# Performance work log

Measured on AMD Instinct MI355X. Metric: run time of the kernel, lower is better.

The kernel has to match this reference:

```python
import jax, jax.numpy as jnp
import numpy as np

BN_EPS = 1e-5
B, N, C, PART = 2, 4096, 128, 50


def _bn(h, g, b):
    # eval-mode BatchNorm1d with fresh-init running stats (mean=0, var=1)
    s = g / jnp.sqrt(1.0 + BN_EPS)
    return h * s[:, None] + b[:, None]


def _conv(w, h):
    # Conv1d kernel_size=1: [O,Cin] x [B,Cin,N] -> [B,O,N]
    return jnp.einsum('oc,bcn->bon', w, h)


def _sa(h, qk_w, v_w, v_b, t_w, t_b, g, b):
    q = _conv(qk_w, h)                       # [B,32,N]; k_conv shares q_conv weight -> k == q
    v = _conv(v_w, h) + v_b[:, None]         # [B,C,N]
    energy = jnp.einsum('bcn,bcm->bnm', q, q)  # [B,N,N]
    att = jax.nn.softmax(energy, axis=-1)
    att = att / (1e-9 + att.sum(axis=1, keepdims=True))  # L1 renorm over columns
    x_r = jnp.einsum('bcn,bnm->bcm', v, att)  # [B,C,N]
    x_r = jax.nn.relu(_bn(_conv(t_w, h - x_r) + t_b[:, None], g, b))
    return h + x_r


def setup_inputs() -> dict:
    key = jax.random.key(0)
    ks = jax.random.split(key, 16)
    d = {
        'x': jax.random.normal(ks[0], (B, N, 3), jnp.float32),
        'cls_label': jax.random.uniform(ks[1], (B, 16, 1), jnp.float32),
        'conv1_w': jax.random.normal(ks[2], (128, 3), jnp.float32) * 0.3,
        'bn1_g': jnp.ones((128,), jnp.float32), 'bn1_b': jnp.zeros((128,), jnp.float32),
        'conv2_w': jax.random.normal(ks[3], (128, 128), jnp.float32) * 0.08,
        'bn2_g': jnp.ones((128,), jnp.float32), 'bn2_b': jnp.zeros((128,), jnp.float32),
        'sa_qk_w': jax.random.normal(ks[4], (4, 32, 128), jnp.float32) * 0.08,
        'sa_v_w': jax.random.normal(ks[5], (4, 128, 128), jnp.float32) * 0.08,
        'sa_v_b': jnp.zeros((4, 128), jnp.float32),
        'sa_t_w': jax.random.normal(ks[6], (4, 128, 128), jnp.float32) * 0.08,
        'sa_t_b': jnp.zeros((4, 128), jnp.float32),
        'sa_bn_g': jnp.ones((4, 128), jnp.float32), 'sa_bn_b': jnp.zeros((4, 128), jnp.float32),
        'fuse_w': jax.random.normal(ks[7], (1024, 512), jnp.float32) * 0.04,
        'fuse_bn_g': jnp.ones((1024,), jnp.float32), 'fuse_bn_b': jnp.zeros((1024,), jnp.float32),
        'label_w': jax.random.normal(ks[8], (64, 16), jnp.float32) * 0.25,
        'label_bn_g': jnp.ones((64,), jnp.float32), 'label_bn_b': jnp.zeros((64,), jnp.float32),
        'convs1_w': jax.random.normal(ks[9], (512, 3136), jnp.float32) * 0.018,
        'convs1_b': jnp.zeros((512,), jnp.float32),
        'bns1_g': jnp.ones((512,), jnp.float32), 'bns1_b': jnp.zeros((512,), jnp.float32),
        'convs2_w': jax.random.normal(ks[10], (256, 512), jnp.float32) * 0.04,
        'convs2_b': jnp.zeros((256,), jnp.float32),
        'bns2_g': jnp.ones((256,), jnp.float32), 'bns2_b': jnp.zeros((256,), jnp.float32),
        'convs3_w': jax.random.normal(ks[11], (50, 256), jnp.float32) * 0.06,
        'convs3_b': jnp.zeros((50,), jnp.float32),
    }
    return d


def reference(x, cls_label, conv1_w, bn1_g, bn1_b, conv2_w, bn2_g, bn2_b,
              sa_qk_w, sa_v_w, sa_v_b, sa_t_w, sa_t_b, sa_bn_g, sa_bn_b,
              fuse_w, fuse_bn_g, fuse_bn_b, label_w, label_bn_g, label_bn_b,
              convs1_w, convs1_b, bns1_g, bns1_b, convs2_w, convs2_b, bns2_g, bns2_b,
              convs3_w, convs3_b):
    h = jnp.transpose(x, (0, 2, 1))                      # [B,3,N]
    h = jax.nn.relu(_bn(_conv(conv1_w, h), bn1_g, bn1_b))
    h = jax.nn.relu(_bn(_conv(conv2_w, h), bn2_g, bn2_b))
    feats = []
    for i in range(4):
        h = _sa(h, sa_qk_w[i], sa_v_w[i], sa_v_b[i], sa_t_w[i], sa_t_b[i], sa_bn_g[i], sa_bn_b[i])
        feats.append(h)
    h = jnp.concatenate(feats, axis=1)                   # [B,512,N]
    h = jax.nn.leaky_relu(_bn(_conv(fuse_w, h), fuse_bn_g, fuse_bn_b), 0.2)  # [B,1024,N]
    x_max = jnp.max(h, axis=2, keepdims=True)            # [B,1024,1]
    x_avg = jnp.mean(h, axis=2, keepdims=True)
    cls_f = jax.nn.leaky_relu(_bn(_conv(label_w, cls_label), label_bn_g, label_bn_b), 0.2)  # [B,64,1]
    n = h.shape[2]
    glob = jnp.concatenate([
        jnp.broadcast_to(x_max, (h.shape[0], 1024, n)),
        jnp.broadcast_to(x_avg, (h.shape[0], 1024, n)),
        jnp.broadcast_to(cls_f, (h.shape[0], 64, n)),
    ], axis=1)
    h = jnp.concatenate([h, glob], axis=1)               # [B,3136,N]
    h = jax.nn.relu(_bn(_conv(convs1_w, h) + convs1_b[:, None], bns1_g, bns1_b))
    # dropout is identity in eval mode
    h = jax.nn.relu(_bn(_conv(convs2_w, h) + convs2_b[:, None], bns2_g, bns2_b))
    h = _conv(convs3_w, h) + convs3_b[:, None]           # [B,50,N]
    return h
```

## Files before the change

### kernel.cpp

```cpp
#include <hip/hip_runtime.h>

#define NP 4096
#define BB 2

typedef __attribute__((ext_vector_type(8))) short short8;
typedef __attribute__((ext_vector_type(4))) float f32x4;
#define MFMA_BF16 __builtin_amdgcn_mfma_f32_16x16x32_bf16

__device__ __forceinline__ float wsum(float v){
  #pragma unroll
  for (int o = 32; o; o >>= 1) v += __shfl_down(v, o, 64);
  return v;
}
__device__ __forceinline__ unsigned short f2bf(float x){
  unsigned int u = __float_as_uint(x);
  return (unsigned short)((u + 0x7fffu + ((u >> 16) & 1u)) >> 16);
}
__device__ __forceinline__ float bfh(unsigned short h){
  return __uint_as_float((unsigned int)h << 16);
}
__device__ __forceinline__ float bf2f(unsigned short h, unsigned short l){
  return bfh(h) + bfh(l);
}
__device__ __forceinline__ short8 ld8(const unsigned short* p){
  return *(const short8*)p;
}

__global__ __launch_bounds__(256) void k_wsplit(
    const float* __restrict__ src, size_t src_ls,
    unsigned short* __restrict__ dh, unsigned short* __restrict__ dl,
    size_t dst_ls, int O, int O_span, int O_pad, int o_base, int Cin, int ldsrc)
{
  const int y = blockIdx.y;
  const int idx = blockIdx.x * 256 + threadIdx.x;
  const int chunks = (Cin >> 6) * O_span * 8;
  if (idx >= chunks) return;
  const int qs = idx & 7;
  const int ol = (idx >> 3) % O_span;
  const int cc = idx / (8 * O_span);
  const int od = o_base + ol;
  short8 vh = {0,0,0,0,0,0,0,0}, vl = {0,0,0,0,0,0,0,0};
  if (ol < O) {
    const float* sp = src + (size_t)y * src_ls + (size_t)ol * ldsrc
                    + cc * 64 + ((qs ^ (od & 7)) << 3);
    const float4 a = *(const float4*)sp;
    const float4 c = *(const float4*)(sp + 4);
    float wv[8] = {a.x,a.y,a.z,a.w,c.x,c.y,c.z,c.w};
    #pragma unroll
    for (int j = 0; j < 8; ++j) {
      const unsigned short hh = f2bf(wv[j]);
      vh[j] = (short)hh;
      vl[j] = (short)f2bf(wv[j] - bfh(hh));
    }
  }
  const size_t d = ((size_t)cc * O_pad + od) * 64 + qs * 8;
  *(short8*)&dh[(size_t)y * dst_ls + d] = vh;
  *(short8*)&dl[(size_t)y * dst_ls + d] = vl;
}

__global__ __launch_bounds__(256) void k_conv1(
    const float* __restrict__ x, const float* __restrict__ w,
    const float* __restrict__ g, const float* __restrict__ bb,
    unsigned short* __restrict__ h0h, unsigned short* __restrict__ h0l)
{
  const int tid = threadIdx.x;
  const int n = blockIdx.x * 32 + (tid >> 3);
  const int oc = (tid & 7) * 16;
  const int b = blockIdx.y;
  const float x0 = x[((size_t)b * NP + n) * 3 + 0];
  const float x1 = x[((size_t)b * NP + n) * 3 + 1];
  const float x2 = x[((size_t)b * NP + n) * 3 + 2];
  const size_t base = ((size_t)b * NP + n) * 128 + oc;
  #pragma unroll
  for (int half = 0; half < 2; ++half) {
    short8 vh, vl;
    #pragma unroll
    for (int j = 0; j < 8; ++j) {
      const int o = oc + half * 8 + j;
      float v = w[o*3]*x0 + w[o*3+1]*x1 + w[o*3+2]*x2;
      v = v * (g[o] * rsqrtf(1.f + 1e-5f)) + bb[o];
      v = fmaxf(v, 0.f);
      const unsigned short hh = f2bf(v);
      vh[j] = (short)hh;
      vl[j] = (short)f2bf(v - bfh(hh));
    }
    *(short8*)&h0h[base + half * 8] = vh;
    *(short8*)&h0l[base + half * 8] = vl;
  }
}

template<int ACT, bool BN, bool RES, bool CNBF, int OT, int NT, bool QV = false>
__global__ __launch_bounds__(256) void k_mm(
    const unsigned short* __restrict__ Ah, const unsigned short* __restrict__ Al,
    int ldA, size_t A_bs,
    const unsigned short* __restrict__ Whp, const unsigned short* __restrict__ Wlp,
    int O_pad,
    const float* __restrict__ convb, int convb_bs,
    const float* __restrict__ bng, const float* __restrict__ bnb,
    const unsigned short* __restrict__ Rh, const unsigned short* __restrict__ Rl,
    int ldR, size_t R_bs,
    unsigned short* __restrict__ Onh, unsigned short* __restrict__ Onl,
    int ldON, size_t ON_bs,
    float* __restrict__ Ocn, size_t OCN_bs,
    int O, int Cin)
{
  constexpr int OF = OT / 16;
  constexpr int NTILES = NP / (NT * 64);
  constexpr int CHK = NTILES / 8;
  constexpr int STR = OF * 16 + 8;
  constexpr int LW_US = OT * 64;
  constexpr int ST_US = 64 * STR;
  constexpr int SM_US = (4*LW_US > 2*ST_US) ? 4*LW_US : 2*ST_US;
  constexpr int PW = OT / 32;

  const int bid = blockIdx.x;
  const int j  = bid >> 3;
  const int nt = (bid & 7) * CHK + (j % CHK);
  const int o0 = (j / CHK) * OT;
  const int n0 = nt * (NT * 64);
  const int b  = blockIdx.y;
  const int tid = threadIdx.x;
  const int w = tid >> 6, lane = tid & 63, lo = lane & 15, hi = lane >> 4;

  __shared__ __align__(16) unsigned short smem[SM_US];
  unsigned short* sTh = smem;
  unsigned short* sTl = smem + ST_US;

  const unsigned short* Ahb = Ah + (size_t)b * A_bs;
  const unsigned short* Alb = Al + (size_t)b * A_bs;

  f32x4 acc[NT][OF];
  #pragma unroll
  for (int nf = 0; nf < NT; ++nf)
    #pragma unroll
    for (int of = 0; of < OF; ++of) acc[nf][of] = (f32x4){0.f,0.f,0.f,0.f};

  const int nw = n0 + w * (NT * 16);

  short8 wrh[PW], wrl[PW];
  {
    const size_t wb = (size_t)o0 * 64;
    #pragma unroll
    for (int q = 0; q < PW; ++q) {
      const int cid = tid + q * 256;
      wrh[q] = ld8(Whp + wb + (size_t)cid * 8);
      wrl[q] = ld8(Wlp + wb + (size_t)cid * 8);
    }
  }

  for (int c0 = 0; c0 < Cin; c0 += 64) {
    const int p = (c0 >> 6) & 1;
    unsigned short* bWh = smem + p * 2 * LW_US;
    unsigned short* bWl = bWh + LW_US;
    #pragma unroll
    for (int q = 0; q < PW; ++q) {
      const int cid = tid + q * 256;
      *(short8*)&bWh[cid * 8] = wrh[q];
      *(short8*)&bWl[cid * 8] = wrl[q];
    }
    if (c0 + 64 < Cin) {
      const size_t wb = ((size_t)((c0 >> 6) + 1) * O_pad + o0) * 64;
      #pragma unroll
      for (int q = 0; q < PW; ++q) {
        const int cid = tid + q * 256;
        wrh[q] = ld8(Whp + wb + (size_t)cid * 8);
        wrl[q] = ld8(Wlp + wb + (size_t)cid * 8);
      }
    }
    __syncthreads();
    #pragma unroll
    for (int ks = 0; ks < 2; ++ks) {
      short8 ah[NT], al[NT];
      #pragma unroll
      for (int nf = 0; nf < NT; ++nf) {
        const int n = nw + nf * 16 + lo;
        const size_t idx = (size_t)n * ldA + c0 + ks * 32 + hi * 8;
        ah[nf] = ld8(Ahb + idx);
        al[nf] = ld8(Alb + idx);
      }
      #pragma unroll
      for (int of = 0; of < OF; ++of) {
        const int row = of * 16 + lo;
        const int qs = (ks * 4 + hi) ^ (row & 7);
        const short8 bh = ld8(&bWh[row * 64 + qs * 8]);
        const short8 bl = ld8(&bWl[row * 64 + qs * 8]);
        #pragma unroll
        for (int nf = 0; nf < NT; ++nf) {
          acc[nf][of] = MFMA_BF16(ah[nf], bh, acc[nf][of], 0, 0, 0);
          acc[nf][of] = MFMA_BF16(ah[nf], bl, acc[nf][of], 0, 0, 0);
          acc[nf][of] = MFMA_BF16(al[nf], bh, acc[nf][of], 0, 0, 0);
        }
      }
    }
  }

  if (Ocn && (!QV || o0 >= 32)) {
    #pragma unroll
    for (int of = 0; of < OF; ++of) {
      const int o = o0 + of * 16 + lo;
      if (o < O) {
        const int oe = QV ? (o - 32) : o;
        const float cb = convb ? convb[(size_t)b * convb_bs + oe] : 0.f;
        float sg = 0.f, sb = 0.f;
        if (BN) { sg = bng[oe] * rsqrtf(1.f + 1e-5f); sb = bnb[oe]; }
        #pragma unroll
        for (int nf = 0; nf < NT; ++nf) {
          const int n = nw + nf * 16 + hi * 4;
          float vv[4];
          #pragma unroll
          for (int r = 0; r < 4; ++r) {
            float v = acc[nf][of][r] + cb;
            if (BN) v = v * sg + sb;
            if (ACT == 1) v = fmaxf(v, 0.f);
            if (ACT == 2) v = v > 0.f ? v : 0.2f * v;
            vv[r] = v;
          }
          if (CNBF) {
            ushort4 pk;
            pk.x = f2bf(vv[0]); pk.y = f2bf(vv[1]);
            pk.z = f2bf(vv[2]); pk.w = f2bf(vv[3]);
            *(ushort4*)&((unsigned short*)Ocn)[(size_t)b * OCN_bs + (size_t)oe * NP + n] = pk;
          } else {
            *(float4*)&Ocn[(size_t)b * OCN_bs + (size_t)oe * NP + n] =
                make_float4(vv[0], vv[1], vv[2], vv[3]);
          }
        }
      }
    }
  }

  if (Onh && (!QV || o0 == 0)) {
    #pragma unroll
    for (int nf = 0; nf < NT; ++nf) {
      __syncthreads();
      #pragma unroll
      for (int of = 0; of < OF; ++of) {
        const int o = o0 + of * 16 + lo;
        const float cb = (convb && !QV) ? convb[(size_t)b * convb_bs + o] : 0.f;
        float sg = 0.f, sb = 0.f;
        if (BN) { sg = bng[o] * rsqrtf(1.f + 1e-5f); sb = bnb[o]; }
        #pragma unroll
        for (int r = 0; r < 4; ++r) {
          float v = acc[nf][of][r] + cb;
          if (BN) v = v * sg + sb;
          if (ACT == 1) v = fmaxf(v, 0.f);
          if (ACT == 2) v = v > 0.f ? v : 0.2f * v;
          const int lrow = w * 16 + hi * 4 + r;
          const unsigned short hh = f2bf(v);
          sTh[lrow * STR + of * 16 + lo] = hh;
          sTl[lrow * STR + of * 16 + lo] = f2bf(v - bfh(hh));
        }
      }
      __syncthreads();
      for (int c = tid; c < 64 * OF * 2; c += 256) {
        const int lrow = c / (OF * 2);
        const int oc = (c % (OF * 2)) * 8;
        const int n = n0 + (lrow >> 4) * (NT * 16) + nf * 16 + (lrow & 15);
        const int o = o0 + oc;
        short8 hv = *(short8*)&sTh[lrow * STR + oc];
        short8 lv = *(short8*)&sTl[lrow * STR + oc];
        if (RES) {
          const short8 rhv = ld8(Rh + (size_t)b * R_bs + (size_t)n * ldR + o);
          const short8 rlv = ld8(Rl + (size_t)b * R_bs + (size_t)n * ldR + o);
          #pragma unroll
          for (int jj = 0; jj < 8; ++jj) {
            float v = bf2f((unsigned short)hv[jj], (unsigned short)lv[jj])
                    + bf2f((unsigned short)rhv[jj], (unsigned short)rlv[jj]);
            const unsigned short hh2 = f2bf(v);
            hv[jj] = (short)hh2;
            lv[jj] = (short)f2bf(v - bfh(hh2));
          }
        }
        *(short8*)&Onh[(size_t)b * ON_bs + (size_t)n * ldON + o] = hv;
        *(short8*)&Onl[(size_t)b * ON_bs + (size_t)n * ldON + o] = lv;
      }
    }
  }
}

__global__ __launch_bounds__(256) void k_passA(
    const unsigned short* __restrict__ qh, const unsigned short* __restrict__ ql,
    float* __restrict__ pmax, float* __restrict__ psum)
{
  const int m0 = blockIdx.x * 64;
  const int ns = blockIdx.y;
  const int b  = blockIdx.z;
  const int tid = threadIdx.x;
  const int w = tid >> 6, lane = tid & 63, lo = lane & 15, hi = lane >> 4;
  const unsigned short* qhb = qh + (size_t)b * NP * 32;
  const unsigned short* qlb = ql + (size_t)b * NP * 32;

  short8 bh[4], bl[4];
  #pragma unroll
  for (int fj = 0; fj < 4; ++fj) {
    const int m = m0 + fj * 16 + lo;
    bh[fj] = ld8(qhb + (size_t)m * 32 + hi * 8);
    bl[fj] = ld8(qlb + (size_t)m * 32 + hi * 8);
  }
  float mx[4], sm[4];
  #pragma unroll
  for (int fj = 0; fj < 4; ++fj) { mx[fj] = -3e38f; sm[fj] = 0.f; }

  const int nbeg = ns * 512;
  for (int ch = 0; ch < 8; ++ch) {
    const int n0 = nbeg + ch * 64;
    const int nr = n0 + w * 16 + lo;
    const short8 ah = ld8(qhb + (size_t)nr * 32 + hi * 8);
    const short8 al = ld8(qlb + (size_t)nr * 32 + hi * 8);
    #pragma unroll
    for (int fj = 0; fj < 4; ++fj) {
      f32x4 e = MFMA_BF16(ah, bh[fj], (f32x4){0.f,0.f,0.f,0.f}, 0, 0, 0);
      e = MFMA_BF16(ah, bl[fj], e, 0, 0, 0);
      e = MFMA_BF16(al, bh[fj], e, 0, 0, 0);
      const float lm = fmaxf(fmaxf(e[0], e[1]), fmaxf(e[2], e[3]));
      const float nm = fmaxf(mx[fj], lm);
      sm[fj] = sm[fj] * __expf(mx[fj] - nm)
             + __expf(e[0]-nm) + __expf(e[1]-nm) + __expf(e[2]-nm) + __expf(e[3]-nm);
      mx[fj] = nm;
    }
  }
  #pragma unroll
  for (int fj = 0; fj < 4; ++fj) {
    #pragma unroll
    for (int off = 16; off <= 32; off <<= 1) {
      const float om = __shfl_down(mx[fj], off, 64);
      const float os = __shfl_down(sm[fj], off, 64);
      const float nm = fmaxf(mx[fj], om);
      sm[fj] = sm[fj] * __expf(mx[fj] - nm) + os * __expf(om - nm);
      mx[fj] = nm;
    }
  }
  __shared__ float wmx[4][64], wsm[4][64];
  if (hi == 0) {
    #pragma unroll
    for (int fj = 0; fj < 4; ++fj) {
      wmx[w][fj * 16 + lo] = mx[fj];
      wsm[w][fj * 16 + lo] = sm[fj];
    }
  }
  __syncthreads();
  if (tid < 64) {
    float fm = wmx[0][tid], fs = wsm[0][tid];
    #pragma unroll
    for (int w2 = 1; w2 < 4; ++w2) {
      const float om = wmx[w2][tid], os = wsm[w2][tid];
      const float nm = fmaxf(fm, om);
      fs = fs * __expf(fm - nm) + os * __expf(om - nm);
      fm = nm;
    }
    pmax[((size_t)b * 8 + ns) * NP + m0 + tid] = fm;
    psum[((size_t)b * 8 + ns) * NP + m0 + tid] = fs;
  }
}

__global__ __launch_bounds__(256) void k_passB(
    const unsigned short* __restrict__ qh, const unsigned short* __restrict__ ql,
    const unsigned short* __restrict__ vbf,
    const float* __restrict__ pmax, const float* __restrict__ psum,
    float* __restrict__ ypart, float* __restrict__ csp)
{
  const int m0 = blockIdx.x * 64;
  const int ns = blockIdx.y;
  const int b  = blockIdx.z;
  const int tid = threadIdx.x;
  const int w = tid >> 6, lane = tid & 63, lo = lane & 15, hi = lane >> 4;
  const unsigned short* qhb = qh + (size_t)b * NP * 32;
  const unsigned short* qlb = ql + (size_t)b * NP * 32;
  const unsigned short* vbb = vbf + (size_t)b * 128 * NP;

  __shared__ __align__(16) unsigned short Pt[2][64 * 64];
  __shared__ float csred[4][64];
  __shared__ float rm_l[1024], ri_l[1024];

  const int nbeg = ns * 1024;
  {
    const int n4 = tid * 4;
    #pragma unroll
    for (int k = 0; k < 4; ++k) {
      const int n = nbeg + n4 + k;
      float mx = -3e38f;
      #pragma unroll
      for (int s = 0; s < 8; ++s)
        mx = fmaxf(mx, pmax[((size_t)b*8 + s) * NP + n]);
      float sm = 0.f;
      #pragma unroll
      for (int s = 0; s < 8; ++s)
        sm += psum[((size_t)b*8 + s) * NP + n] * __expf(pmax[((size_t)b*8 + s) * NP + n] - mx);
      rm_l[n4 + k] = mx;
      ri_l[n4 + k] = 1.f / sm;
    }
  }

  short8 bh[4], bl[4];
  #pragma unroll
  for (int fj = 0; fj < 4; ++fj) {
    const int m = m0 + fj * 16 + lo;
    bh[fj] = ld8(qhb + (size_t)m * 32 + hi * 8);
    bl[fj] = ld8(qlb + (size_t)m * 32 + hi * 8);
  }
  f32x4 yacc[2][4];
  #pragma unroll
  for (int cf = 0; cf < 2; ++cf)
    #pragma unroll
    for (int fj = 0; fj < 4; ++fj) yacc[cf][fj] = (f32x4){0.f,0.f,0.f,0.f};
  float cs[4] = {0.f, 0.f, 0.f, 0.f};

  const int swz = (lo & 7) << 3;
  const int c0 = w * 32;
  __syncthreads();
  for (int ch = 0; ch < 16; ++ch) {
    unsigned short* Ptc = &Pt[ch & 1][0];
    const int n0 = nbeg + ch * 64;
    const int nr = n0 + w * 16 + lo;
    const short8 ah = ld8(qhb + (size_t)nr * 32 + hi * 8);
    const short8 al = ld8(qlb + (size_t)nr * 32 + hi * 8);
    f32x4 e[4];
    #pragma unroll
    for (int fj = 0; fj < 4; ++fj) {
      e[fj] = MFMA_BF16(ah, bh[fj], (f32x4){0.f,0.f,0.f,0.f}, 0, 0, 0);
      e[fj] = MFMA_BF16(ah, bl[fj], e[fj], 0, 0, 0);
      e[fj] = MFMA_BF16(al, bh[fj], e[fj], 0, 0, 0);
    }
    float rmv[4], riv[4];
    #pragma unroll
    for (int r = 0; r < 4; ++r) {
      const int nl = ch * 64 + w * 16 + hi * 4 + r;
      rmv[r] = rm_l[nl];
      riv[r] = ri_l[nl];
    }
    #pragma unroll
    for (int fj = 0; fj < 4; ++fj) {
      float p[4];
      #pragma unroll
      for (int r = 0; r < 4; ++r) p[r] = __expf(e[fj][r] - rmv[r]) * riv[r];
      cs[fj] += p[0] + p[1] + p[2] + p[3];
      ushort4 pk;
      pk.x = f2bf(p[0]); pk.y = f2bf(p[1]); pk.z = f2bf(p[2]); pk.w = f2bf(p[3]);
      const int row = fj * 16 + lo;
      const int col = (w * 16 + hi * 4) ^ swz;
      *(ushort4*)&Ptc[row * 64 + col] = pk;
    }
    short8 vfrag[2][2];
    #pragma unroll
    for (int cf = 0; cf < 2; ++cf)
      #pragma unroll
      for (int ks = 0; ks < 2; ++ks)
        vfrag[cf][ks] = ld8(vbb + (size_t)(c0 + cf*16 + lo) * NP + n0 + ks*32 + hi*8);
    __syncthreads();
    #pragma unroll
    for (int ks = 0; ks < 2; ++ks) {
      #pragma unroll
      for (int fj = 0; fj < 4; ++fj) {
        const int row = fj * 16 + lo;
        const int col = (ks * 32 + hi * 8) ^ swz;
        const short8 pf = ld8(&Ptc[row * 64 + col]);
        #pragma unroll
        for (int cf = 0; cf < 2; ++cf)
          yacc[cf][fj] = MFMA_BF16(vfrag[cf][ks], pf, yacc[cf][fj], 0, 0, 0);
      }
    }
  }
  float* yp = ypart + ((size_t)b * 4 + ns) * NP * 128;
  #pragma unroll
  for (int cf = 0; cf < 2; ++cf)
    #pragma unroll
    for (int fj = 0; fj < 4; ++fj) {
      const int m = m0 + fj * 16 + lo;
      const int c = w * 32 + cf * 16 + hi * 4;
      *(f32x4*)&yp[(size_t)m * 128 + c] = yacc[cf][fj];
    }
  #pragma unroll
  for (int fj = 0; fj < 4; ++fj) {
    cs[fj] += __shfl_down(cs[fj], 16, 64);
    cs[fj] += __shfl_down(cs[fj], 32, 64);
  }
  __syncthreads();
  if (hi == 0) {
    #pragma unroll
    for (int fj = 0; fj < 4; ++fj) csred[w][fj * 16 + lo] = cs[fj];
  }
  __syncthreads();
  if (tid < 64)
    csp[((size_t)b * 4 + ns) * NP + m0 + tid] =
        csred[0][tid] + csred[1][tid] + csred[2][tid] + csred[3][tid];
}

__global__ __launch_bounds__(256) void k_combineB(
    const float* __restrict__ ypart, const float* __restrict__ csp,
    const unsigned short* __restrict__ hinh, const unsigned short* __restrict__ hinl,
    int ldH, size_t H_bs,
    unsigned short* __restrict__ dh, unsigned short* __restrict__ dl)
{
  const size_t i = (size_t)blockIdx.x * 256 + threadIdx.x;
  const int c = (int)(i & 127);
  const int n = (int)((i >> 7) & (NP - 1));
  const int b = (int)(i >> 19);
  float s = 1e-9f, y = 0.f;
  #pragma unroll
  for (int ns = 0; ns < 4; ++ns) {
    y += ypart[(((size_t)b*4 + ns) * NP + n) * 128 + c];
    s += csp[((size_t)b*4 + ns) * NP + n];
  }
  const float h = bf2f(hinh[(size_t)b * H_bs + (size_t)n * ldH + c],
                       hinl[(size_t)b * H_bs + (size_t)n * ldH + c]);
  const float d = h - y / s;
  const unsigned short hh = f2bf(d);
  dh[i] = hh;
  dl[i] = f2bf(d - bfh(hh));
}

__global__ __launch_bounds__(256) void k_maxavg_p(
    const unsigned short* __restrict__ fh, const unsigned short* __restrict__ fl,
    float* __restrict__ pmx, float* __restrict__ psm)
{
  const int tid = threadIdx.x;
  const int c4 = (tid & 15) * 4;
  const int st = tid >> 4;
  const int o0 = blockIdx.x * 64;
  const int nsp = blockIdx.y;
  const int b = blockIdx.z;
  const int nbeg = nsp * 256;
  const unsigned short* fhb = fh + (size_t)b * NP * 1024 + o0 + c4;
  const unsigned short* flb = fl + (size_t)b * NP * 1024 + o0 + c4;
  float mx[4] = {-3e38f,-3e38f,-3e38f,-3e38f}, sm[4] = {0.f,0.f,0.f,0.f};
  #pragma unroll 4
  for (int n = nbeg + st; n < nbeg + 256; n += 16) {
    const ushort4 vh = *(const ushort4*)(fhb + (size_t)n * 1024);
    const ushort4 vl = *(const ushort4*)(flb + (size_t)n * 1024);
    const float v0 = bf2f(vh.x, vl.x), v1 = bf2f(vh.y, vl.y);
    const float v2 = bf2f(vh.z, vl.z), v3 = bf2f(vh.w, vl.w);
    mx[0] = fmaxf(mx[0], v0); sm[0] += v0;
    mx[1] = fmaxf(mx[1], v1); sm[1] += v1;
    mx[2] = fmaxf(mx[2], v2); sm[2] += v2;
    mx[3] = fmaxf(mx[3], v3); sm[3] += v3;
  }
  __shared__ float smx[16][64], ssm[16][64];
  #pragma unroll
  for (int j = 0; j < 4; ++j) { smx[st][c4 + j] = mx[j]; ssm[st][c4 + j] = sm[j]; }
  __syncthreads();
  if (tid < 64) {
    float m = -3e38f, s = 0.f;
    #pragma unroll
    for (int k = 0; k < 16; ++k) { m = fmaxf(m, smx[k][tid]); s += ssm[k][tid]; }
    pmx[((size_t)b * 16 + nsp) * 1024 + o0 + tid] = m;
    psm[((size_t)b * 16 + nsp) * 1024 + o0 + tid] = s;
  }
}

__global__ __launch_bounds__(256) void k_maxavg_c(
    const float* __restrict__ pmx, const float* __restrict__ psm,
    float* __restrict__ xm, float* __restrict__ xa)
{
  const int i = blockIdx.x * 256 + threadIdx.x;
  const int c = i & 1023;
  const int b = i >> 10;
  float m = -3e38f, s = 0.f;
  #pragma unroll
  for (int k = 0; k < 16; ++k) {
    m = fmaxf(m, pmx[((size_t)b * 16 + k) * 1024 + c]);
    s += psm[((size_t)b * 16 + k) * 1024 + c];
  }
  xm[i] = m;
  xa[i] = s * (1.f / NP);
}

__global__ void k_cls(const float* __restrict__ cl, const float* __restrict__ W,
                      const float* __restrict__ g, const float* __restrict__ bb,
                      float* __restrict__ clsf)
{
  const int t = threadIdx.x;
  const int b = t >> 6, o = t & 63;
  float a = 0.f;
  #pragma unroll
  for (int j = 0; j < 16; ++j) a += W[o * 16 + j] * cl[b * 16 + j];
  a = a * (g[o] * rsqrtf(1.f + 1e-5f)) + bb[o];
  clsf[b * 64 + o] = a > 0.f ? a : 0.2f * a;
}

__global__ __launch_bounds__(256) void k_gbias(
    const float* __restrict__ W1, const float* __restrict__ xm,
    const float* __restrict__ xa, const float* __restrict__ clsf,
    const float* __restrict__ c1b, float* __restrict__ gb)
{
  const int o = blockIdx.x, b = blockIdx.y;
  float a = 0.f;
  for (int j = threadIdx.x; j < 2112; j += 256) {
    const float gv = (j < 1024) ? xm[b * 1024 + j]
                   : (j < 2048) ? xa[b * 1024 + (j - 1024)]
                                : clsf[b * 64 + (j - 2048)];
    a += W1[(size_t)o * 3136 + 1024 + j] * gv;
  }
  a = wsum(a);
  __shared__ float red[4];
  const int w = threadIdx.x >> 6;
  if ((threadIdx.x & 63) == 0) red[w] = a;
  __syncthreads();
  if (threadIdx.x == 0) gb[b * 512 + o] = red[0] + red[1] + red[2] + red[3] + c1b[o];
}

extern "C" void kernel_launch(void* const* d_in, const int* in_sizes, int n_in,
                              void* d_out, int out_size, void* d_ws, size_t ws_size,
                              hipStream_t stream)
{
  const float* x        = (const float*)d_in[0];
  const float* cls_lab  = (const float*)d_in[1];
  const float* conv1_w  = (const float*)d_in[2];
  const float* bn1_g    = (const float*)d_in[3];
  const float* bn1_b    = (const float*)d_in[4];
  const float* conv2_w  = (const float*)d_in[5];
  const float* bn2_g    = (const float*)d_in[6];
  const float* bn2_b    = (const float*)d_in[7];
  const float* sa_qk_w  = (const float*)d_in[8];
  const float* sa_v_w   = (const float*)d_in[9];
  const float* sa_v_b   = (const float*)d_in[10];
  const float* sa_t_w   = (const float*)d_in[11];
  const float* sa_t_b   = (const float*)d_in[12];
  const float* sa_bn_g  = (const float*)d_in[13];
  const float* sa_bn_b  = (const float*)d_in[14];
  const float* fuse_w   = (const float*)d_in[15];
  const float* fuse_g   = (const float*)d_in[16];
  const float* fuse_b   = (const float*)d_in[17];
  const float* label_w  = (const float*)d_in[18];
  const float* label_g  = (const float*)d_in[19];
  const float* label_b  = (const float*)d_in[20];
  const float* c1_w     = (const float*)d_in[21];
  const float* c1_b     = (const float*)d_in[22];
  const float* bns1_g   = (const float*)d_in[23];
  const float* bns1_b   = (const float*)d_in[24];
  const float* c2_w     = (const float*)d_in[25];
  const float* c2_b     = (const float*)d_in[26];
  const float* bns2_g   = (const float*)d_in[27];
  const float* bns2_b   = (const float*)d_in[28];
  const float* c3_w     = (const float*)d_in[29];
  const float* c3_b     = (const float*)d_in[30];
  float* outp = (float*)d_out;

  float* f = (float*)d_ws;
  size_t off = 0;
  auto us = [&](size_t n_ushort) { unsigned short* p = (unsigned short*)(f + off);
                                   off += (n_ushort + 1) / 2; return p; };
  unsigned short* h0h  = us((size_t)BB*NP*128);
  unsigned short* h0l  = us((size_t)BB*NP*128);
  unsigned short* h1h  = us((size_t)BB*NP*128);
  unsigned short* h1l  = us((size_t)BB*NP*128);
  unsigned short* hch  = us((size_t)BB*NP*512);
  unsigned short* hcl  = us((size_t)BB*NP*512);
  unsigned short* qTh  = us((size_t)BB*NP*32);
  unsigned short* qTl  = us((size_t)BB*NP*32);
  unsigned short* vb   = us((size_t)BB*128*NP);
  unsigned short* dhb  = us((size_t)BB*NP*128);
  unsigned short* dlb  = us((size_t)BB*NP*128);
  unsigned short* wc2h = us(2*128*64);        unsigned short* wc2l = us(2*128*64);
  unsigned short* wqvh = us(4*2*160*64);      unsigned short* wqvl = us(4*2*160*64);
  unsigned short* wth  = us(4*2*128*64);      unsigned short* wtl  = us(4*2*128*64);
  unsigned short* wfh  = us(8*1024*64);       unsigned short* wfl  = us(8*1024*64);
  unsigned short* w1h  = us(16*512*64);       unsigned short* w1l  = us(16*512*64);
  unsigned short* w2h  = us(8*256*64);        unsigned short* w2l  = us(8*256*64);
  unsigned short* w3h  = us(4*64*64);         unsigned short* w3l  = us(4*64*64);
  float* pmax  = f + off; off += (size_t)BB*8*NP;
  float* psum  = f + off; off += (size_t)BB*8*NP;
  float* csp   = f + off; off += (size_t)BB*4*NP;
  float* pmx   = f + off; off += (size_t)BB*16*1024;
  float* psm   = f + off; off += (size_t)BB*16*1024;
  float* xm    = f + off; off += (size_t)BB*1024;
  float* xa    = f + off; off += (size_t)BB*1024;
  float* clsf  = f + off; off += (size_t)BB*64;
  float* gb    = f + off; off += (size_t)BB*512;
  off = (off + 255) & ~(size_t)255;
  float* ypart = f + off;
  unsigned short* fuh = (unsigned short*)ypart;
  unsigned short* ful = fuh + (size_t)BB*NP*1024;
  unsigned short* o1h = ful + (size_t)BB*NP*1024;
  unsigned short* o1l = o1h + (size_t)BB*NP*512;
  unsigned short* o2h = o1l + (size_t)BB*NP*512;
  unsigned short* o2l = o2h + (size_t)BB*NP*256;

  const dim3 blk(256);

  k_wsplit<<<dim3(8,1),   blk, 0, stream>>>(conv2_w, 0, wc2h, wc2l, 0, 128, 128, 128, 0, 128, 128);
  k_wsplit<<<dim3(2,4),   blk, 0, stream>>>(sa_qk_w, 32*128, wqvh, wqvl, 2*160*64, 32, 32, 160, 0, 128, 128);
  k_wsplit<<<dim3(8,4),   blk, 0, stream>>>(sa_v_w, 128*128, wqvh, wqvl, 2*160*64, 128, 128, 160, 32, 128, 128);
  k_wsplit<<<dim3(8,4),   blk, 0, stream>>>(sa_t_w, 128*128, wth, wtl, 2*128*64, 128, 128, 128, 0, 128, 128);
  k_wsplit<<<dim3(256,1), blk, 0, stream>>>(fuse_w, 0, wfh, wfl, 0, 1024, 1024, 1024, 0, 512, 512);
  k_wsplit<<<dim3(256,1), blk, 0, stream>>>(c1_w, 0, w1h, w1l, 0, 512, 512, 512, 0, 1024, 3136);
  k_wsplit<<<dim3(64,1),  blk, 0, stream>>>(c2_w, 0, w2h, w2l, 0, 256, 256, 256, 0, 512, 512);
  k_wsplit<<<dim3(8,1),   blk, 0, stream>>>(c3_w, 0, w3h, w3l, 0, 50, 64, 64, 0, 256, 256);

  k_conv1<<<dim3(128, BB), blk, 0, stream>>>(x, conv1_w, bn1_g, bn1_b, h0h, h0l);

  k_mm<1,true,false,false,32,1><<<dim3(256,BB), blk, 0, stream>>>(
      h0h, h0l, 128, (size_t)NP*128, wc2h, wc2l, 128, nullptr, 0, bn2_g, bn2_b,
      nullptr, nullptr, 0, 0, h1h, h1l, 128, (size_t)NP*128, nullptr, 0, 128, 128);

  for (int i = 0; i < 4; ++i) {
    const unsigned short* hinh = (i == 0) ? h1h : hch + (size_t)(i-1)*128;
    const unsigned short* hinl = (i == 0) ? h1l : hcl + (size_t)(i-1)*128;
    const int ldH = (i == 0) ? 128 : 512;
    const size_t H_bs = (size_t)NP * ldH;

    k_mm<0,false,false,true,32,1,true><<<dim3(320,BB), blk, 0, stream>>>(
        hinh, hinl, ldH, H_bs, wqvh + (size_t)i*2*160*64, wqvl + (size_t)i*2*160*64, 160,
        sa_v_b + (size_t)i*128, 0, nullptr, nullptr,
        nullptr, nullptr, 0, 0,
        qTh, qTl, 32, (size_t)NP*32,
        (float*)vb, (size_t)128*NP, 160, 128);

    k_passA<<<dim3(64,8,BB), blk, 0, stream>>>(qTh, qTl, pmax, psum);
    k_passB<<<dim3(64,4,BB), blk, 0, stream>>>(qTh, qTl, vb, pmax, psum, ypart, csp);
    k_combineB<<<dim3(BB*NP*128/256), blk, 0, stream>>>(
        ypart, csp, hinh, hinl, ldH, H_bs, dhb, dlb);

    k_mm<1,true,true,false,32,1><<<dim3(256,BB), blk, 0, stream>>>(
        dhb, dlb, 128, (size_t)NP*128, wth + (size_t)i*2*128*64, wtl + (size_t)i*2*128*64, 128,
        sa_t_b + (size_t)i*128, 0, sa_bn_g + (size_t)i*128, sa_bn_b + (size_t)i*128,
        hinh, hinl, ldH, H_bs,
        hch + (size_t)i*128, hcl + (size_t)i*128, 512, (size_t)NP*512,
        nullptr, 0, 128, 128);
  }

  k_mm<2,true,false,false,64,2><<<dim3(512,BB), blk, 0, stream>>>(
      hch, hcl, 512, (size_t)NP*512, wfh, wfl, 1024, nullptr, 0, fuse_g, fuse_b,
      nullptr, nullptr, 0, 0, fuh, ful, 1024, (size_t)NP*1024, nullptr, 0, 1024, 512);

  k_maxavg_p<<<dim3(16,16,BB), blk, 0, stream>>>(fuh, ful, pmx, psm);
  k_maxavg_c<<<dim3(BB*1024/256), blk, 0, stream>>>(pmx, psm, xm, xa);
  k_cls<<<dim3(1), dim3(128), 0, stream>>>(cls_lab, label_w, label_g, label_b, clsf);
  k_gbias<<<dim3(512, BB), blk, 0, stream>>>(c1_w, xm, xa, clsf, c1_b, gb);

  k_mm<1,true,false,false,64,2><<<dim3(256,BB), blk, 0, stream>>>(
      fuh, ful, 1024, (size_t)NP*1024, w1h, w1l, 512, gb, 512, bns1_g, bns1_b,
      nullptr, nullptr, 0, 0, o1h, o1l, 512, (size_t)NP*512, nullptr, 0, 512, 1024);

  k_mm<1,true,false,false,64,1><<<dim3(256,BB), blk, 0, stream>>>(
      o1h, o1l, 512, (size_t)NP*512, w2h, w2l, 256, c2_b, 0, bns2_g, bns2_b,
      nullptr, nullptr, 0, 0, o2h, o2l, 256, (size_t)NP*256, nullptr, 0, 256, 512);

  k_mm<0,false,false,false,64,1><<<dim3(64,BB), blk, 0, stream>>>(
      o2h, o2l, 256, (size_t)NP*256, w3h, w3l, 64, c3_b, 0, nullptr, nullptr,
      nullptr, nullptr, 0, 0, nullptr, nullptr, 0, 0,
      outp, (size_t)50*NP, 50, 256);
}
```

Before: 419.1 us.

## Software-pipeline A-operand global loads one chunk ahead in conv GEMM

The channel loop is restructured into a two-chunk unrolled pipeline. The next chunk's activation fragments (hi/lo bf16) are prefetched into registers while the current chunk's MFMAs run, alongside the existing weight prefetch. This is meant to hide global load latency for the A operand, which was previously loaded right before use. The extra register sets raise VGPR pressure and may reduce occupancy. The loop also assumes Cin/64 is even, and the cc+1 load is unguarded.

```diff
diff --git a/kernel.cpp b/kernel.cpp
--- a/kernel.cpp
+++ b/kernel.cpp
@@ -138,61 +138,84 @@
   const int nw = n0 + w * (NT * 16);
 
   short8 wrh[PW], wrl[PW];
-  {
-    const size_t wb = (size_t)o0 * 64;
+  short8 a0h[2][NT], a0l[2][NT], a1h[2][NT], a1l[2][NT];
+
+  auto loadW = [&](int ci) {
+    const size_t wb = ((size_t)ci * O_pad + o0) * 64;
     #pragma unroll
     for (int q = 0; q < PW; ++q) {
       const int cid = tid + q * 256;
       wrh[q] = ld8(Whp + wb + (size_t)cid * 8);
       wrl[q] = ld8(Wlp + wb + (size_t)cid * 8);
     }
-  }
-
-  for (int c0 = 0; c0 < Cin; c0 += 64) {
-    const int p = (c0 >> 6) & 1;
-    unsigned short* bWh = smem + p * 2 * LW_US;
-    unsigned short* bWl = bWh + LW_US;
+  };
+  auto writeW = [&](unsigned short* bWh, unsigned short* bWl) {
     #pragma unroll
     for (int q = 0; q < PW; ++q) {
       const int cid = tid + q * 256;
       *(short8*)&bWh[cid * 8] = wrh[q];
       *(short8*)&bWl[cid * 8] = wrl[q];
     }
-    if (c0 + 64 < Cin) {
-      const size_t wb = ((size_t)((c0 >> 6) + 1) * O_pad + o0) * 64;
-      #pragma unroll
-      for (int q = 0; q < PW; ++q) {
-        const int cid = tid + q * 256;
-        wrh[q] = ld8(Whp + wb + (size_t)cid * 8);
-        wrl[q] = ld8(Wlp + wb + (size_t)cid * 8);
+  };
+
+#define LOAD_A(AH, AL, C0)                                             \
+  { _Pragma("unroll")                                                  \
+    for (int ks = 0; ks < 2; ++ks) {                                   \
+      _Pragma("unroll")                                                \
+      for (int nf = 0; nf < NT; ++nf) {                                \
+        const int n = nw + nf * 16 + lo;                               \
+        const size_t idx = (size_t)n * ldA + (C0) + ks * 32 + hi * 8;  \
+        AH[ks][nf] = ld8(Ahb + idx);                                   \
+        AL[ks][nf] = ld8(Alb + idx);                                   \
+      }                                                                \
+    } }
+
+#define COMPUTE(BWH, BWL, AHc, ALc)                                    \
+  { _Pragma("unroll")                                                  \
+    for (int ks = 0; ks < 2; ++ks) {                                   \
+      _Pragma("unroll")                                                \
+      for (int of = 0; of < OF; ++of) {                                \
+        const int row = of * 16 + lo;                                  \
+        const int qs = (ks * 4 + hi) ^ (row & 7);                      \
+        const short8 bh = ld8(&(BWH)[row * 64 + qs * 8]);              \
+        const short8 bl = ld8(&(BWL)[row * 64 + qs * 8]);              \
+        _Pragma("unroll")                                              \
+        for (int nf = 0; nf < NT; ++nf) {                              \
+          acc[nf][of] = MFMA_BF16(AHc[ks][nf], bh, acc[nf][of], 0,0,0);\
+          acc[nf][of] = MFMA_BF16(AHc[ks][nf], bl, acc[nf][of], 0,0,0);\
+          acc[nf][of] = MFMA_BF16(ALc[ks][nf], bh, acc[nf][of], 0,0,0);\
+        }                                                              \
+      }                                                                \
+    } }
+
+  loadW(0);
+  LOAD_A(a0h, a0l, 0);
+
+  const int nch = Cin >> 6;
+  for (int cc = 0; cc < nch; cc += 2) {
+    {
+      unsigned short* bWh = smem;
+      unsigned short* bWl = smem + LW_US;
+      writeW(bWh, bWl);
+      loadW(cc + 1);
+      LOAD_A(a1h, a1l, (cc + 1) * 64);
+      __syncthreads();
+      COMPUTE(bWh, bWl, a0h, a0l);
+    }
+    {
+      unsigned short* bWh = smem + 2 * LW_US;
+      unsigned short* bWl = bWh + LW_US;
+      writeW(bWh, bWl);
+      if (cc + 2 < nch) {
+        loadW(cc + 2);
+        LOAD_A(a0h, a0l, (cc + 2) * 64);
       }
-    }
-    __syncthreads();
-    #pragma unroll
-    for (int ks = 0; ks < 2; ++ks) {
-      short8 ah[NT], al[NT];
-      #pragma unroll
-      for (int nf = 0; nf < NT; ++nf) {
-        const int n = nw + nf * 16 + lo;
-        const size_t idx = (size_t)n * ldA + c0 + ks * 32 + hi * 8;
-        ah[nf] = ld8(Ahb + idx);
-        al[nf] = ld8(Alb + idx);
-      }
-      #pragma unroll
-      for (int of = 0; of < OF; ++of) {
-        const int row = of * 16 + lo;
-        const int qs = (ks * 4 + hi) ^ (row & 7);
-        const short8 bh = ld8(&bWh[row * 64 + qs * 8]);
-        const short8 bl = ld8(&bWl[row * 64 + qs * 8]);
-        #pragma unroll
-        for (int nf = 0; nf < NT; ++nf) {
-          acc[nf][of] = MFMA_BF16(ah[nf], bh, acc[nf][of], 0, 0, 0);
-          acc[nf][of] = MFMA_BF16(ah[nf], bl, acc[nf][of], 0, 0, 0);
-          acc[nf][of] = MFMA_BF16(al[nf], bh, acc[nf][of], 0, 0, 0);
-        }
-      }
-    }
-  }
+      __syncthreads();
+      COMPUTE(bWh, bWl, a1h, a1l);
+    }
+  }
+#undef LOAD_A
+#undef COMPUTE
 
   if (Ocn && (!QV || o0 >= 32)) {
     #pragma unroll
```

After: 417.9 us. Within noise of the previous version (-0.3%).
